# Kernel tuning notes

Measured on AMD Instinct MI355X. Metric: run time of the kernel, lower is better.

The kernel has to match this reference:

```python
import jax, jax.numpy as jnp
import numpy as np

N = 10000
F_IN, F_HID, F_OUT = 128, 64, 32
E = 320000
MAX_LOGSTD = 10.0


def _glorot(key, fan_in, fan_out):
    lim = np.sqrt(6.0 / (fan_in + fan_out))
    return jax.random.uniform(key, (fan_in, fan_out), jnp.float32, -lim, lim)


def setup_inputs() -> dict:
    key = jax.random.key(0)
    ks = jax.random.split(key, 8)
    x = jax.random.normal(ks[0], (N, F_IN), jnp.float32)
    edge_index = jax.random.randint(ks[1], (2, E), 0, N, jnp.int64)
    eps = jax.random.normal(ks[2], (N, F_OUT), jnp.float32)
    return {
        'x': x,
        'edge_index': edge_index,
        'eps': eps,
        'W0': _glorot(ks[3], F_IN, F_HID), 'b0': jnp.zeros((F_HID,), jnp.float32),
        'W1': _glorot(ks[4], F_HID, F_HID), 'b1': jnp.zeros((F_HID,), jnp.float32),
        'Wmu': _glorot(ks[5], F_HID, F_OUT), 'bmu': jnp.zeros((F_OUT,), jnp.float32),
        'Wls': _glorot(ks[6], F_HID, F_OUT), 'bls': jnp.zeros((F_OUT,), jnp.float32),
    }


def _gcn_norm(edge_index, n):
    # add self-loops, symmetric normalization (PyG gcn_norm, improved=False)
    loop = jnp.arange(n, dtype=edge_index.dtype)
    src = jnp.concatenate([edge_index[0], loop])
    dst = jnp.concatenate([edge_index[1], loop])
    deg = jax.ops.segment_sum(jnp.ones_like(src, jnp.float32), dst, num_segments=n)
    dinv = jnp.where(deg > 0, deg ** -0.5, 0.0)
    norm = dinv[src] * dinv[dst]  # [E+N]
    return src, dst, norm


def _gcn_conv(x, W, b, src, dst, norm, n):
    h = x @ W                              # [N, Fo] dense transform
    m = norm[:, None] * h[src]             # per-edge gather + scale
    return jax.ops.segment_sum(m, dst, num_segments=n) + b  # scatter-add


def reference(x, edge_index, eps, W0, b0, W1, b1, Wmu, bmu, Wls, bls):
    n = x.shape[0]
    src, dst, norm = _gcn_norm(edge_index, n)
    h = jax.nn.relu(_gcn_conv(x, W0, b0, src, dst, norm, n))
    h = jax.nn.relu(_gcn_conv(h, W1, b1, src, dst, norm, n))
    mu = _gcn_conv(h, Wmu, bmu, src, dst, norm, n)
    logstd = jnp.minimum(_gcn_conv(h, Wls, bls, src, dst, norm, n), MAX_LOGSTD)
    z = mu + eps * jnp.exp(logstd)         # VGAE reparameterize (training mode)
    adj_pred = jax.nn.sigmoid(z @ z.T)     # InnerProductDecoder.forward_all
    return adj_pred
```

## Files before the change

kernel.cpp:

```cpp
#include <hip/hip_runtime.h>
#include <math.h>

#define NN 10000
#define EE 320000
#define FIN 128
#define FHID 64
#define FOUT 32

typedef float f32x4 __attribute__((ext_vector_type(4)));


__global__ void k_count(const int* __restrict__ dst, int* __restrict__ deg, int E) {
    int e = blockIdx.x * blockDim.x + threadIdx.x;
    if (e < E) atomicAdd(&deg[dst[e]], 1);
}

__global__ void k_scan(const int* __restrict__ cnt, int* __restrict__ rowptr,
                       float* __restrict__ dinv, int n) {
    __shared__ int buf[256];
    __shared__ int carry_s;
    if (threadIdx.x == 0) carry_s = 0;
    __syncthreads();
    int nC = (n + 255) / 256;
    for (int c = 0; c < nC; ++c) {
        int i = c * 256 + threadIdx.x;
        int v = (i < n) ? cnt[i] : 0;
        if (i < n) dinv[i] = rsqrtf((float)v + 1.0f);
        buf[threadIdx.x] = v;
        __syncthreads();
        for (int off = 1; off < 256; off <<= 1) {
            int o = (threadIdx.x >= off) ? buf[threadIdx.x - off] : 0;
            __syncthreads();
            buf[threadIdx.x] += o;
            __syncthreads();
        }
        int incl = buf[threadIdx.x];
        int carry = carry_s;
        if (i < n) rowptr[i] = carry + incl - v;
        __syncthreads();
        if (threadIdx.x == 255) carry_s = carry + incl;
        __syncthreads();
    }
    if (threadIdx.x == 0) rowptr[n] = carry_s;
}

__global__ void k_fill(const int* __restrict__ src, const int* __restrict__ dst,
                       const float* __restrict__ dinv, const int* __restrict__ rowptr,
                       int* __restrict__ fillcnt, int2* __restrict__ csr, int E) {
    int e = blockIdx.x * blockDim.x + threadIdx.x;
    if (e >= E) return;
    int s = src[e], d = dst[e];
    float w = dinv[s] * dinv[d];
    int pos = rowptr[d] + atomicAdd(&fillcnt[d], 1);
    csr[pos] = make_int2(s, __float_as_int(w));
}


template<int K, int CAT>
__global__ __launch_bounds__(256) void k_xform(const float* __restrict__ in,
                                               const float* __restrict__ Wa,
                                               const float* __restrict__ Wb,
                                               float* __restrict__ out, int n) {
    __shared__ float Ws[K * 64];
    if (CAT) {
        for (int i = threadIdx.x; i < 64 * 64; i += 256) {
            int k = i >> 6, j = i & 63;
            Ws[i] = (j < 32) ? Wa[k * 32 + j] : Wb[k * 32 + (j - 32)];
        }
    } else {
        for (int i = threadIdx.x; i < K * 64; i += 256) Ws[i] = Wa[i];
    }
    __syncthreads();
    int lane = threadIdx.x & 63;
    int wv = threadIdx.x >> 6;
#pragma unroll
    for (int r = 0; r < 4; ++r) {
        int row = blockIdx.x * 16 + wv * 4 + r;
        if (row >= n) continue;
        const float* xr = in + (long long)row * K;
        float xa = xr[lane];
        float xb = (K > 64) ? xr[(K > 64 ? 64 : 0) + lane] : 0.0f;
        float acc = 0.0f;
#pragma unroll
        for (int k = 0; k < K; ++k) {
            float xk = (k < 64) ? __shfl(xa, k) : __shfl(xb, k - 64);
            acc += xk * Ws[k * 64 + lane];
        }
        out[(long long)row * 64 + lane] = acc;
    }
}


template<int MODE>
__global__ __launch_bounds__(256) void k_prop(const float* __restrict__ t,
                                              const int2* __restrict__ csr,
                                              const int* __restrict__ rowptr,
                                              const float* __restrict__ dinv,
                                              const float* __restrict__ ba,
                                              const float* __restrict__ bb,
                                              const float* __restrict__ eps,
                                              float* __restrict__ out, int n) {
    int lane = threadIdx.x & 63;
    int node = blockIdx.x * (blockDim.x >> 6) + (threadIdx.x >> 6);
    if (node >= n) return;
    float di = dinv[node];
    float acc = di * di * t[(long long)node * 64 + lane];
    int e = rowptr[node], end = rowptr[node + 1];
    for (; e < end; ++e) {
        int2 ed = csr[e];
        acc += __int_as_float(ed.y) * t[(long long)ed.x * 64 + lane];
    }
    if (MODE == 0) {
        out[(long long)node * 64 + lane] = fmaxf(acc + ba[lane], 0.0f);
    } else {
        float v = acc + ((lane < 32) ? ba[lane] : bb[lane - 32]);
        float ls = __shfl(v, lane | 32);
        if (lane < 32) {
            float zv = v + eps[(long long)node * 32 + lane] * __expf(fminf(ls, 10.0f));
            out[(long long)node * 32 + lane] = zv;
        }
    }
}


__global__ __launch_bounds__(256) void k_decoder(const float* __restrict__ z,
                                                 float* __restrict__ out, int n) {
    __shared__ float ziT[32][132];
    __shared__ float zjT[32][132];
    int i0 = blockIdx.y * 128;
    int j0 = blockIdx.x * 128;
    int t = threadIdx.x;
#pragma unroll
    for (int r = 0; r < 4; ++r) {
        int idx = t + r * 256;
        int row = idx >> 3;
        int c4 = (idx & 7) << 2;
        float4 vi = make_float4(0.f, 0.f, 0.f, 0.f);
        float4 vj = make_float4(0.f, 0.f, 0.f, 0.f);
        if (i0 + row < n) vi = *(const float4*)&z[(long long)(i0 + row) * 32 + c4];
        if (j0 + row < n) vj = *(const float4*)&z[(long long)(j0 + row) * 32 + c4];
        ziT[c4 + 0][row] = vi.x; ziT[c4 + 1][row] = vi.y;
        ziT[c4 + 2][row] = vi.z; ziT[c4 + 3][row] = vi.w;
        zjT[c4 + 0][row] = vj.x; zjT[c4 + 1][row] = vj.y;
        zjT[c4 + 2][row] = vj.z; zjT[c4 + 3][row] = vj.w;
    }
    __syncthreads();

    int tr = t >> 4, tc = t & 15;
    int rbase = tr * 8, cbase = tc * 8;
    float acc[8][8];
#pragma unroll
    for (int u = 0; u < 8; ++u)
#pragma unroll
        for (int v = 0; v < 8; ++v) acc[u][v] = 0.0f;

#pragma unroll 4
    for (int k = 0; k < 32; ++k) {
        float4 a0 = *(const float4*)&ziT[k][rbase];
        float4 a1 = *(const float4*)&ziT[k][rbase + 4];
        float4 b0v = *(const float4*)&zjT[k][cbase];
        float4 b1v = *(const float4*)&zjT[k][cbase + 4];
        float a[8] = {a0.x, a0.y, a0.z, a0.w, a1.x, a1.y, a1.z, a1.w};
        float b[8] = {b0v.x, b0v.y, b0v.z, b0v.w, b1v.x, b1v.y, b1v.z, b1v.w};
#pragma unroll
        for (int u = 0; u < 8; ++u)
#pragma unroll
            for (int v = 0; v < 8; ++v)
                acc[u][v] += a[u] * b[v];
    }

#pragma unroll
    for (int u = 0; u < 8; ++u) {
        int gi = i0 + rbase + u;
        if (gi < n) {
            float r[8];
#pragma unroll
            for (int v = 0; v < 8; ++v)
                r[v] = __fdividef(1.0f, 1.0f + __expf(-acc[u][v]));
            long long base = (long long)gi * n + (j0 + cbase);
            if (j0 + cbase + 8 <= n) {
                f32x4 lo = {r[0], r[1], r[2], r[3]};
                f32x4 hi = {r[4], r[5], r[6], r[7]};
                __builtin_nontemporal_store(lo, (f32x4*)&out[base]);
                __builtin_nontemporal_store(hi, (f32x4*)&out[base + 4]);
            } else {
#pragma unroll
                for (int v = 0; v < 8; ++v)
                    if (j0 + cbase + v < n) out[base + v] = r[v];
            }
        }
    }
}


extern "C" void kernel_launch(void* const* d_in, const int* in_sizes, int n_in,
                              void* d_out, int out_size, void* d_ws, size_t ws_size,
                              hipStream_t stream) {
    const float* x   = (const float*)d_in[0];
    const int*   ei  = (const int*)d_in[1];
    const float* eps = (const float*)d_in[2];
    const float* W0  = (const float*)d_in[3];
    const float* b0  = (const float*)d_in[4];
    const float* W1  = (const float*)d_in[5];
    const float* b1  = (const float*)d_in[6];
    const float* Wmu = (const float*)d_in[7];
    const float* bmu = (const float*)d_in[8];
    const float* Wls = (const float*)d_in[9];
    const float* bls = (const float*)d_in[10];
    float* out = (float*)d_out;

    int E = in_sizes[1] / 2;
    int n = in_sizes[0] / FIN;

    char* ws = (char*)d_ws;
    int*   deg    = (int*)(ws + 0);
    float* dinv   = (float*)(ws + 40960);
    int*   rowptr = (int*)(ws + 81920);
    int2*  csr    = (int2*)(ws + 122880);
    float* bufA   = (float*)(ws + 2682880);
    float* bufB   = (float*)(ws + 5242880);
    float* z      = (float*)(ws + 7802880);

    const int* src = ei;
    const int* dst = ei + E;

    (void)hipMemsetAsync(deg, 0, n * sizeof(int), stream);
    k_count<<<(E + 255) / 256, 256, 0, stream>>>(dst, deg, E);
    k_scan<<<1, 256, 0, stream>>>(deg, rowptr, dinv, n);
    (void)hipMemsetAsync(deg, 0, n * sizeof(int), stream);
    k_fill<<<(E + 255) / 256, 256, 0, stream>>>(src, dst, dinv, rowptr, deg, csr, E);

    int xblocks = (n + 15) / 16;
    int pblocks = (n + 3) / 4;
    k_xform<128, 0><<<xblocks, 256, 0, stream>>>(x, W0, nullptr, bufA, n);
    k_prop<0><<<pblocks, 256, 0, stream>>>(bufA, csr, rowptr, dinv, b0, nullptr, nullptr, bufB, n);
    k_xform<64, 0><<<xblocks, 256, 0, stream>>>(bufB, W1, nullptr, bufA, n);
    k_prop<0><<<pblocks, 256, 0, stream>>>(bufA, csr, rowptr, dinv, b1, nullptr, nullptr, bufB, n);
    k_xform<64, 1><<<xblocks, 256, 0, stream>>>(bufB, Wmu, Wls, bufA, n);
    k_prop<1><<<pblocks, 256, 0, stream>>>(bufA, csr, rowptr, dinv, bmu, bls, eps, z, n);

    int nt = (n + 127) / 128;
    dim3 g(nt, nt);
    k_decoder<<<g, 256, 0, stream>>>(z, out, n);
}
```

Before: 707.8 us.

## Parallelize CSR scan, batch edge loads in propagation, use cached output stores

Replaces the single-block serial prefix scan with a two-stage scan: one block computes per-chunk offsets, then a multi-block pass scans each chunk. The two memsets become one by giving the fill counter its own buffer. The propagation kernel now loads up to 64 CSR entries cooperatively per wavefront and broadcasts them with shuffles, instead of each lane loading every edge. The decoder's nontemporal stores become ordinary float4 stores, which may change how the 400 MB output moves through the cache. The prescan assumes at most 64 chunks, so it only holds for n up to 16384.

```diff
diff --git a/kernel.cpp b/kernel.cpp
--- a/kernel.cpp
+++ b/kernel.cpp
@@ -1,11 +1,7 @@
 #include <hip/hip_runtime.h>
 #include <math.h>
 
-#define NN 10000
-#define EE 320000
 #define FIN 128
-#define FHID 64
-#define FOUT 32
 
 typedef float f32x4 __attribute__((ext_vector_type(4)));
 
@@ -15,33 +11,51 @@
     if (e < E) atomicAdd(&deg[dst[e]], 1);
 }
 
-__global__ void k_scan(const int* __restrict__ cnt, int* __restrict__ rowptr,
-                       float* __restrict__ dinv, int n) {
+__global__ __launch_bounds__(256) void k_prescan(const int* __restrict__ deg,
+                                                 int* __restrict__ boff,
+                                                 int* __restrict__ rowptr, int n) {
+    __shared__ int bs[64];
+    int NB = (n + 255) >> 8;
+    int c = threadIdx.x;
+    if (c < 64) {
+        int s = 0;
+        if (c < NB) {
+            int base = c << 8;
+            int lim = n - base; if (lim > 256) lim = 256;
+            for (int i = 0; i < lim; ++i) s += deg[base + i];
+        }
+        bs[c] = s;
+    }
+    __syncthreads();
+    if (threadIdx.x < 64) {
+        int v = bs[threadIdx.x];
+        int incl = v;
+        for (int off = 1; off < 64; off <<= 1) {
+            int o = __shfl_up(incl, off);
+            if ((int)threadIdx.x >= off) incl += o;
+        }
+        if ((int)threadIdx.x < NB) boff[threadIdx.x] = incl - v;
+        if (threadIdx.x == 63) rowptr[n] = incl;
+    }
+}
+
+__global__ __launch_bounds__(256) void k_scatter(const int* __restrict__ deg,
+                                                 const int* __restrict__ boff,
+                                                 int* __restrict__ rowptr,
+                                                 float* __restrict__ dinv, int n) {
     __shared__ int buf[256];
-    __shared__ int carry_s;
-    if (threadIdx.x == 0) carry_s = 0;
-    __syncthreads();
-    int nC = (n + 255) / 256;
-    for (int c = 0; c < nC; ++c) {
-        int i = c * 256 + threadIdx.x;
-        int v = (i < n) ? cnt[i] : 0;
-        if (i < n) dinv[i] = rsqrtf((float)v + 1.0f);
-        buf[threadIdx.x] = v;
+    int i = blockIdx.x * 256 + threadIdx.x;
+    int v = (i < n) ? deg[i] : 0;
+    if (i < n) dinv[i] = rsqrtf((float)v + 1.0f);
+    buf[threadIdx.x] = v;
+    __syncthreads();
+    for (int off = 1; off < 256; off <<= 1) {
+        int o = (threadIdx.x >= off) ? buf[threadIdx.x - off] : 0;
         __syncthreads();
-        for (int off = 1; off < 256; off <<= 1) {
-            int o = (threadIdx.x >= off) ? buf[threadIdx.x - off] : 0;
-            __syncthreads();
-            buf[threadIdx.x] += o;
-            __syncthreads();
-        }
-        int incl = buf[threadIdx.x];
-        int carry = carry_s;
-        if (i < n) rowptr[i] = carry + incl - v;
+        buf[threadIdx.x] += o;
         __syncthreads();
-        if (threadIdx.x == 255) carry_s = carry + incl;
-        __syncthreads();
-    }
-    if (threadIdx.x == 0) rowptr[n] = carry_s;
+    }
+    if (i < n) rowptr[i] = boff[blockIdx.x] + buf[threadIdx.x] - v;
 }
 
 __global__ void k_fill(const int* __restrict__ src, const int* __restrict__ dst,
@@ -101,14 +115,20 @@
                                               const float* __restrict__ eps,
                                               float* __restrict__ out, int n) {
     int lane = threadIdx.x & 63;
-    int node = blockIdx.x * (blockDim.x >> 6) + (threadIdx.x >> 6);
+    int node = blockIdx.x * 4 + (threadIdx.x >> 6);
     if (node >= n) return;
     float di = dinv[node];
     float acc = di * di * t[(long long)node * 64 + lane];
-    int e = rowptr[node], end = rowptr[node + 1];
-    for (; e < end; ++e) {
-        int2 ed = csr[e];
-        acc += __int_as_float(ed.y) * t[(long long)ed.x * 64 + lane];
+    int e0 = rowptr[node], e1 = rowptr[node + 1];
+    for (int base = e0; base < e1; base += 64) {
+        int m = e1 - base; if (m > 64) m = 64;
+        int2 my = make_int2(0, 0);
+        if (lane < m) my = csr[base + lane];
+        for (int i = 0; i < m; ++i) {
+            int s = __shfl(my.x, i);
+            float w = __int_as_float(__shfl(my.y, i));
+            acc += w * t[(long long)s * 64 + lane];
+        }
     }
     if (MODE == 0) {
         out[(long long)node * 64 + lane] = fmaxf(acc + ba[lane], 0.0f);
@@ -179,10 +199,8 @@
                 r[v] = __fdividef(1.0f, 1.0f + __expf(-acc[u][v]));
             long long base = (long long)gi * n + (j0 + cbase);
             if (j0 + cbase + 8 <= n) {
-                f32x4 lo = {r[0], r[1], r[2], r[3]};
-                f32x4 hi = {r[4], r[5], r[6], r[7]};
-                __builtin_nontemporal_store(lo, (f32x4*)&out[base]);
-                __builtin_nontemporal_store(hi, (f32x4*)&out[base + 4]);
+                *(float4*)&out[base]     = make_float4(r[0], r[1], r[2], r[3]);
+                *(float4*)&out[base + 4] = make_float4(r[4], r[5], r[6], r[7]);
             } else {
 #pragma unroll
                 for (int v = 0; v < 8; ++v)
@@ -213,22 +231,25 @@
     int n = in_sizes[0] / FIN;
 
     char* ws = (char*)d_ws;
-    int*   deg    = (int*)(ws + 0);
-    float* dinv   = (float*)(ws + 40960);
-    int*   rowptr = (int*)(ws + 81920);
-    int2*  csr    = (int2*)(ws + 122880);
-    float* bufA   = (float*)(ws + 2682880);
-    float* bufB   = (float*)(ws + 5242880);
-    float* z      = (float*)(ws + 7802880);
+    int*   deg     = (int*)(ws + 0);
+    int*   fillcnt = (int*)(ws + 40960);
+    int*   boff    = (int*)(ws + 81920);
+    int*   rowptr  = (int*)(ws + 82432);
+    float* dinv    = (float*)(ws + 124928);
+    int2*  csr     = (int2*)(ws + 165888);
+    float* bufA    = (float*)(ws + 2725888);
+    float* bufB    = (float*)(ws + 5285888);
+    float* z       = (float*)(ws + 7845888);
 
     const int* src = ei;
     const int* dst = ei + E;
 
-    (void)hipMemsetAsync(deg, 0, n * sizeof(int), stream);
+    (void)hipMemsetAsync(deg, 0, 81920, stream);
     k_count<<<(E + 255) / 256, 256, 0, stream>>>(dst, deg, E);
-    k_scan<<<1, 256, 0, stream>>>(deg, rowptr, dinv, n);
-    (void)hipMemsetAsync(deg, 0, n * sizeof(int), stream);
-    k_fill<<<(E + 255) / 256, 256, 0, stream>>>(src, dst, dinv, rowptr, deg, csr, E);
+    k_prescan<<<1, 256, 0, stream>>>(deg, boff, rowptr, n);
+    int nb = (n + 255) / 256;
+    k_scatter<<<nb, 256, 0, stream>>>(deg, boff, rowptr, dinv, n);
+    k_fill<<<(E + 255) / 256, 256, 0, stream>>>(src, dst, dinv, rowptr, fillcnt, csr, E);
 
     int xblocks = (n + 15) / 16;
     int pblocks = (n + 3) / 4;
```

New measurement: 650.3 us. 8.1% less time.
